# Kernel optimization log

Measured on AMD Instinct MI355X. Metric: run time of the kernel, lower is better.

Reference implementation:

```python
import jax, jax.numpy as jnp
import numpy as np

N_ROWS = 4_194_304  # batch rows
N_LAYERS = 30


def setup_inputs() -> dict:
    key = jax.random.key(0)
    k1, k2, k3, k4, k5 = jax.random.split(key, 5)
    x1 = jax.random.normal(k1, (N_ROWS, 1), dtype=jnp.float32)
    x2 = jax.random.normal(k2, (N_ROWS, 5), dtype=jnp.float32)
    # Per-layer params stacked: Linear(5->1) weight [1,5] + bias [1]; Linear(1->5, no bias) weight [5,1]
    W1 = jax.random.normal(k3, (N_LAYERS, 1, 5), dtype=jnp.float32) * (1.0 / np.sqrt(5.0))
    b1 = jax.random.normal(k4, (N_LAYERS, 1), dtype=jnp.float32) * (1.0 / np.sqrt(5.0))
    W2 = jax.random.normal(k5, (N_LAYERS, 5, 1), dtype=jnp.float32)
    return {"x1": x1, "x2": x2, "W1": W1, "b1": b1, "W2": W2}


def reference(x1, x2, W1, b1, W2):
    # Chain of 30 UpDownDoubleResNetBlock blocks:
    #   x1 = x1 + relu(x2) @ W1^T + b1   (Linear(5,1) with bias)
    #   x2 = x2 + relu(x1) @ W2^T        (Linear(1,5) no bias)
    def step(carry, params):
        h1, h2 = carry
        w1, bb1, w2 = params  # [1,5], [1], [5,1]
        h1 = h1 + jax.nn.relu(h2) @ w1.T + bb1  # [N,1]
        h2 = h2 + jax.nn.relu(h1) @ w2.T        # [N,5]
        return (h1, h2), None

    (x1, x2), _ = jax.lax.scan(step, (x1, x2), (W1, b1, W2))
    return (x1, x2)
```

## Files before the change

kernel.cpp:

```cpp
#include <hip/hip_runtime.h>

#define NL 30

__global__ __launch_bounds__(256) void drn_kernel(
    const float* __restrict__ x1, const float* __restrict__ x2,
    const float* __restrict__ W1, const float* __restrict__ b1,
    const float* __restrict__ W2,
    float* __restrict__ o1, float* __restrict__ o2, int nrows)
{
    __shared__ __align__(16) float sp[NL * 12];
    for (int i = threadIdx.x; i < NL * 12; i += blockDim.x) {
        int l = i / 12, k = i % 12;
        float v = 0.0f;
        if (k < 5)        v = W1[l * 5 + k];
        else if (k == 5)  v = b1[l];
        else if (k < 11)  v = W2[l * 5 + (k - 6)];
        sp[i] = v;
    }
    __syncthreads();

    long t = (long)blockIdx.x * blockDim.x + threadIdx.x;
    long row0 = t * 4;
    if (row0 >= nrows) return;

    float h1[4];
    float h2[20];
    *(float4*)&h1[0] = *(const float4*)(x1 + row0);
    const float4* px2 = (const float4*)(x2 + row0 * 5);
    #pragma unroll
    for (int i = 0; i < 5; ++i) ((float4*)h2)[i] = px2[i];

    for (int l = 0; l < NL; ++l) {
        float4 p0 = *(const float4*)&sp[l * 12];
        float4 p1 = *(const float4*)&sp[l * 12 + 4];
        float4 p2 = *(const float4*)&sp[l * 12 + 8];
        float w1r[5] = {p0.x, p0.y, p0.z, p0.w, p1.x};
        float bb     = p1.y;
        float w2r[5] = {p1.z, p1.w, p2.x, p2.y, p2.z};
        #pragma unroll
        for (int r = 0; r < 4; ++r) {
            float s = bb;
            #pragma unroll
            for (int j = 0; j < 5; ++j)
                s = fmaf(fmaxf(h2[r * 5 + j], 0.0f), w1r[j], s);
            h1[r] += s;
            float rh = fmaxf(h1[r], 0.0f);
            #pragma unroll
            for (int j = 0; j < 5; ++j)
                h2[r * 5 + j] = fmaf(rh, w2r[j], h2[r * 5 + j]);
        }
    }

    *(float4*)(o1 + row0) = *(float4*)&h1[0];
    float4* po2 = (float4*)(o2 + row0 * 5);
    #pragma unroll
    for (int i = 0; i < 5; ++i) po2[i] = ((float4*)h2)[i];
}

extern "C" void kernel_launch(void* const* d_in, const int* in_sizes, int n_in,
                              void* d_out, int out_size, void* d_ws, size_t ws_size,
                              hipStream_t stream) {
    const float* x1 = (const float*)d_in[0];
    const float* x2 = (const float*)d_in[1];
    const float* W1 = (const float*)d_in[2];
    const float* b1 = (const float*)d_in[3];
    const float* W2 = (const float*)d_in[4];
    int nrows = in_sizes[0];
    float* o1 = (float*)d_out;
    float* o2 = (float*)d_out + nrows;

    int nthreads = nrows / 4;
    int block = 256;
    int grid = (nthreads + block - 1) / block;
    drn_kernel<<<grid, block, 0, stream>>>(x1, x2, W1, b1, W2, o1, o2, nrows);
}
```

Before: 205.0 us.

## Rewrite as persistent grid-stride kernel with prefetch, uniform weights, nontemporal IO

Replaces the one-shot kernel with a fixed grid of 2048 blocks. Each thread walks 2-row chunks in a grid-stride loop and prefetches the next chunk's inputs while it computes the current one. Weights are read straight from global memory inside a fully unrolled layer loop, so the compiler can turn them into scalar loads instead of going through shared memory. Loads and stores are nontemporal and occupancy is raised via launch bounds. In exchange, rows per thread drop from 4 to 2, the code relies on nrows dividing evenly (there is no bounds check), and the 30-layer unroll grows code size.

```diff
diff --git a/kernel.cpp b/kernel.cpp
--- a/kernel.cpp
+++ b/kernel.cpp
@@ -2,59 +2,94 @@
 
 #define NL 30
 
-__global__ __launch_bounds__(256) void drn_kernel(
+typedef float f2 __attribute__((ext_vector_type(2)));
+
+__global__ __launch_bounds__(256, 8) void drn_kernel(
     const float* __restrict__ x1, const float* __restrict__ x2,
     const float* __restrict__ W1, const float* __restrict__ b1,
     const float* __restrict__ W2,
-    float* __restrict__ o1, float* __restrict__ o2, int nrows)
+    float* __restrict__ o1, float* __restrict__ o2,
+    int niters, long stride_rows)
 {
-    __shared__ __align__(16) float sp[NL * 12];
-    for (int i = threadIdx.x; i < NL * 12; i += blockDim.x) {
-        int l = i / 12, k = i % 12;
-        float v = 0.0f;
-        if (k < 5)        v = W1[l * 5 + k];
-        else if (k == 5)  v = b1[l];
-        else if (k < 11)  v = W2[l * 5 + (k - 6)];
-        sp[i] = v;
-    }
-    __syncthreads();
+    long row = ((long)blockIdx.x * blockDim.x + threadIdx.x) * 2;
 
-    long t = (long)blockIdx.x * blockDim.x + threadIdx.x;
-    long row0 = t * 4;
-    if (row0 >= nrows) return;
-
-    float h1[4];
-    float h2[20];
-    *(float4*)&h1[0] = *(const float4*)(x1 + row0);
-    const float4* px2 = (const float4*)(x2 + row0 * 5);
-    #pragma unroll
-    for (int i = 0; i < 5; ++i) ((float4*)h2)[i] = px2[i];
-
-    for (int l = 0; l < NL; ++l) {
-        float4 p0 = *(const float4*)&sp[l * 12];
-        float4 p1 = *(const float4*)&sp[l * 12 + 4];
-        float4 p2 = *(const float4*)&sp[l * 12 + 8];
-        float w1r[5] = {p0.x, p0.y, p0.z, p0.w, p1.x};
-        float bb     = p1.y;
-        float w2r[5] = {p1.z, p1.w, p2.x, p2.y, p2.z};
+    f2 c1 = __builtin_nontemporal_load((const f2*)(x1 + row));
+    f2 c2[5];
+    {
+        const f2* p = (const f2*)(x2 + row * 5);
         #pragma unroll
-        for (int r = 0; r < 4; ++r) {
-            float s = bb;
-            #pragma unroll
-            for (int j = 0; j < 5; ++j)
-                s = fmaf(fmaxf(h2[r * 5 + j], 0.0f), w1r[j], s);
-            h1[r] += s;
-            float rh = fmaxf(h1[r], 0.0f);
-            #pragma unroll
-            for (int j = 0; j < 5; ++j)
-                h2[r * 5 + j] = fmaf(rh, w2r[j], h2[r * 5 + j]);
-        }
+        for (int j = 0; j < 5; ++j) c2[j] = __builtin_nontemporal_load(p + j);
     }
 
-    *(float4*)(o1 + row0) = *(float4*)&h1[0];
-    float4* po2 = (float4*)(o2 + row0 * 5);
-    #pragma unroll
-    for (int i = 0; i < 5; ++i) po2[i] = ((float4*)h2)[i];
+    for (int it = 0; it < niters; ++it) {
+        long nrow = row + stride_rows;
+        f2 n1, n2[5];
+        bool has_next = (it + 1 < niters);
+        if (has_next) {
+            n1 = __builtin_nontemporal_load((const f2*)(x1 + nrow));
+            const f2* p = (const f2*)(x2 + nrow * 5);
+            #pragma unroll
+            for (int j = 0; j < 5; ++j) n2[j] = __builtin_nontemporal_load(p + j);
+        }
+
+        float h1a = c1.x, h1b = c1.y;
+        float r0[5] = {c2[0].x, c2[0].y, c2[1].x, c2[1].y, c2[2].x};
+        float r1[5] = {c2[2].y, c2[3].x, c2[3].y, c2[4].x, c2[4].y};
+
+        #pragma unroll
+        for (int l = 0; l < NL; ++l) {
+            float w10 = W1[l * 5 + 0], w11 = W1[l * 5 + 1], w12 = W1[l * 5 + 2],
+                  w13 = W1[l * 5 + 3], w14 = W1[l * 5 + 4];
+            float bb  = b1[l];
+            float w20 = W2[l * 5 + 0], w21 = W2[l * 5 + 1], w22 = W2[l * 5 + 2],
+                  w23 = W2[l * 5 + 3], w24 = W2[l * 5 + 4];
+
+            float s = h1a + bb;
+            s = fmaf(fmaxf(r0[0], 0.f), w10, s);
+            s = fmaf(fmaxf(r0[1], 0.f), w11, s);
+            s = fmaf(fmaxf(r0[2], 0.f), w12, s);
+            s = fmaf(fmaxf(r0[3], 0.f), w13, s);
+            s = fmaf(fmaxf(r0[4], 0.f), w14, s);
+            h1a = s;
+            float rh = fmaxf(s, 0.f);
+            r0[0] = fmaf(rh, w20, r0[0]);
+            r0[1] = fmaf(rh, w21, r0[1]);
+            r0[2] = fmaf(rh, w22, r0[2]);
+            r0[3] = fmaf(rh, w23, r0[3]);
+            r0[4] = fmaf(rh, w24, r0[4]);
+
+            float u = h1b + bb;
+            u = fmaf(fmaxf(r1[0], 0.f), w10, u);
+            u = fmaf(fmaxf(r1[1], 0.f), w11, u);
+            u = fmaf(fmaxf(r1[2], 0.f), w12, u);
+            u = fmaf(fmaxf(r1[3], 0.f), w13, u);
+            u = fmaf(fmaxf(r1[4], 0.f), w14, u);
+            h1b = u;
+            float sh = fmaxf(u, 0.f);
+            r1[0] = fmaf(sh, w20, r1[0]);
+            r1[1] = fmaf(sh, w21, r1[1]);
+            r1[2] = fmaf(sh, w22, r1[2]);
+            r1[3] = fmaf(sh, w23, r1[3]);
+            r1[4] = fmaf(sh, w24, r1[4]);
+        }
+
+        __builtin_nontemporal_store((f2){h1a, h1b}, (f2*)(o1 + row));
+        {
+            f2* p = (f2*)(o2 + row * 5);
+            __builtin_nontemporal_store((f2){r0[0], r0[1]}, p + 0);
+            __builtin_nontemporal_store((f2){r0[2], r0[3]}, p + 1);
+            __builtin_nontemporal_store((f2){r0[4], r1[0]}, p + 2);
+            __builtin_nontemporal_store((f2){r1[1], r1[2]}, p + 3);
+            __builtin_nontemporal_store((f2){r1[3], r1[4]}, p + 4);
+        }
+
+        if (has_next) {
+            c1 = n1;
+            #pragma unroll
+            for (int j = 0; j < 5; ++j) c2[j] = n2[j];
+        }
+        row = nrow;
+    }
 }
 
 extern "C" void kernel_launch(void* const* d_in, const int* in_sizes, int n_in,
@@ -69,8 +104,11 @@
     float* o1 = (float*)d_out;
     float* o2 = (float*)d_out + nrows;
 
-    int nthreads = nrows / 4;
-    int block = 256;
-    int grid = (nthreads + block - 1) / block;
-    drn_kernel<<<grid, block, 0, stream>>>(x1, x2, W1, b1, W2, o1, o2, nrows);
+    const int block = 256;
+    const int grid = 2048;
+    long stride_rows = (long)grid * block * 2;
+    int niters = (int)((nrows + stride_rows - 1) / stride_rows);
+
+    drn_kernel<<<grid, block, 0, stream>>>(x1, x2, W1, b1, W2, o1, o2,
+                                           niters, stride_rows);
 }
```

New measurement: 240.3 us. 1.17x slower.
